# Performance work log

Measured on AMD Instinct MI355X. Metric: run time of the kernel, lower is better.

Reference implementation:

```python
import jax, jax.numpy as jnp
import numpy as np

N_NODES = 100000
N_TYPES = 7
E_PER_TYPE = 250000
D = 128


def setup_inputs() -> dict:
    key = jax.random.key(0)
    k1, k2, k3 = jax.random.split(key, 3)
    x = jax.random.normal(k1, (N_NODES, D), dtype=jnp.float32)
    edge_index = jax.random.randint(k2, (N_TYPES, 2, E_PER_TYPE), 0, N_NODES, dtype=jnp.int64)
    # per-edge-type GNN weights (SwitchModule holds one param set per type)
    W = jax.random.normal(k3, (N_TYPES, D, D), dtype=jnp.float32) * (1.0 / np.sqrt(D))
    b = jnp.zeros((N_TYPES, D), dtype=jnp.float32)
    return {"x": x, "edge_index": edge_index, "W": W, "b": b}


def reference(x, edge_index, W, b):
    # x: [N, D]; edge_index: [T, 2, E]; W: [T, D, D]; b: [T, D]
    N = x.shape[0]
    E = edge_index.shape[-1]
    # per-type linear transform of all node features: [T, N, D]
    h = jnp.einsum('nd,tdf->tnf', x, W) + b[:, None, :]

    def per_type(ht, ei):
        src, dst = ei[0], ei[1]
        msgs = ht[src]                                   # [E, D] gather
        sums = jax.ops.segment_sum(msgs, dst, num_segments=N)
        cnt = jax.ops.segment_sum(jnp.ones((E,), ht.dtype), dst, num_segments=N)
        return sums / jnp.maximum(cnt, 1.0)[:, None]     # mean aggregation

    type_messages = jax.vmap(per_type)(h, edge_index)    # [T, N, D]
    # x_agg = sum(type_messages) / len(type_messages)
    return type_messages.mean(axis=0)
```

## Files before the change

kernel.cpp:

```cpp
#include <hip/hip_runtime.h>


constexpr int NN = 100000;
constexpr int NT = 7;
constexpr int NE = 250000;
constexpr int DD = 128;
constexpr int NROWS = ((NN + 127) / 128) * 128;
constexpr int NPART = 8;
constexpr int PSIZE = (NN + NPART - 1) / NPART;
constexpr int EPB = 1024;
constexpr int NSLAB = (NE + EPB - 1) / EPB;

typedef short bf16x8 __attribute__((ext_vector_type(8)));
typedef float f32x4 __attribute__((ext_vector_type(4)));
typedef int   i32x4 __attribute__((ext_vector_type(4)));
typedef float fltx4 __attribute__((ext_vector_type(4)));

__device__ __forceinline__ unsigned pack_bf16x2(float lo, float hi) {
    unsigned a = __float_as_uint(lo), b = __float_as_uint(hi);
    unsigned al = (a + 0x7FFFu + ((a >> 16) & 1u)) >> 16;
    unsigned bh = (b + 0x7FFFu + ((b >> 16) & 1u)) & 0xFFFF0000u;
    return al | bh;
}

__global__ __launch_bounds__(256) void convx_k(
    const float* __restrict__ x, uint4* __restrict__ xb)
{
    int id = blockIdx.x * 256 + threadIdx.x;
    const fltx4* src = (const fltx4*)x;
    fltx4 v0 = __builtin_nontemporal_load(src + (size_t)id * 2);
    fltx4 v1 = __builtin_nontemporal_load(src + (size_t)id * 2 + 1);
    uint4 o;
    o.x = pack_bf16x2(v0[0], v0[1]);
    o.y = pack_bf16x2(v0[2], v0[3]);
    o.z = pack_bf16x2(v1[0], v1[1]);
    o.w = pack_bf16x2(v1[2], v1[3]);
    xb[id] = o;
}

__global__ __launch_bounds__(256) void wconv_k(
    const float* __restrict__ W, char* __restrict__ WTb)
{
    int wid = (blockIdx.x * 256 + threadIdx.x) >> 6;
    int lane = threadIdx.x & 63;
    int t = wid >> 7, f = wid & 127;
    if (t >= NT) return;
    const float* Wt = W + (size_t)t * DD * DD;
    float w0 = Wt[(size_t)(2 * lane) * DD + f];
    float w1 = Wt[(size_t)(2 * lane + 1) * DD + f];
    int gran = (lane >> 2) ^ (f & 7);
    *(unsigned*)(WTb + (size_t)t * 32768 + f * 256 + gran * 16 + (lane & 3) * 4)
        = pack_bf16x2(w0, w1);
}

__global__ __launch_bounds__(256) void fill_k(
    const int* __restrict__ ei,
    int* __restrict__ cntT,
    int* __restrict__ eslots)
{
    int part = blockIdx.x & (NPART - 1);
    int slab = blockIdx.x >> 3;
    int t = blockIdx.y;
    int e0 = slab * EPB + threadIdx.x * 4;
    if (e0 >= NE) return;
    const int* p = ei + (size_t)t * 2 * NE;
    i32x4 s4 = __builtin_nontemporal_load((const i32x4*)(p + e0));
    i32x4 d4 = __builtin_nontemporal_load((const i32x4*)(p + NE + e0));
    int lo = part * PSIZE;
    int hi = lo + PSIZE;
    int tv = t << 17;
    #pragma unroll
    for (int k = 0; k < 4; ++k) {
        int src = s4[k];
        int dst = d4[k];
        if (dst >= lo && dst < hi) {
            int pos = atomicAdd(cntT + dst, 1);
            if (pos < 64) eslots[(size_t)dst * 64 + pos] = src | tv;
        }
    }
}

__global__ __launch_bounds__(256) void agg_k(
    const char* __restrict__ xb,
    const int* __restrict__ cntT,
    const int* __restrict__ eslots,
    char* __restrict__ aggb,
    unsigned char* __restrict__ bmask,
    int c0, int nc)
{
    int wid = (blockIdx.x * 256 + threadIdx.x) >> 6;
    int lane = threadIdx.x & 63;
    if (wid >= nc) return;
    const int n = c0 + wid;
    const bool live = (n < NN);

    int total = live ? cntT[n] : 0;
    if (total > 64) total = 64;
    int val = (live && lane < total)
            ? __builtin_nontemporal_load(eslots + (size_t)n * 64 + lane) : 0;
    int mytype = (lane < total) ? ((val >> 17) & 7) : 7;

    unsigned long long bal[8];
    #pragma unroll
    for (int t = 0; t < 8; ++t) bal[t] = __ballot(mytype == t);
    int ct[7], st[7];
    {
        int s = 0;
        #pragma unroll
        for (int t = 0; t < 7; ++t) { st[t] = s; ct[t] = (int)__popcll(bal[t]); s += ct[t]; }
    }

    unsigned long long before = 0, mine = bal[7];
    #pragma unroll
    for (int t = 0; t < 7; ++t) {
        before |= (mytype > t) ? bal[t] : 0ull;
        mine = (mytype == t) ? bal[t] : mine;
    }
    int rank = (int)__popcll(before)
             + (int)__popcll(mine & ((1ull << lane) - 1ull));
    int sorted = __builtin_amdgcn_ds_permute(rank << 2, val);
    int val2 = (lane < total) ? (sorted & 0x1FFFF) : NN;

    int gran = (lane >> 2) ^ (wid & 7);
    char* wbase = aggb + (size_t)(wid >> 7) * 32768 + (size_t)(wid & 127) * 256
                + gran * 16 + (lane & 3) * 4;
    const size_t tstride = (size_t)nc * 256;
    unsigned msk = 0;

    #pragma unroll
    for (int tp = 0; tp < 7; tp += 2) {
        const int cA = ct[tp], stA = st[tp];
        const int cB = (tp + 1 < 7) ? ct[tp + 1] : 0;
        const int stB = (tp + 1 < 7) ? st[tp + 1] : 0;
        int m2 = cA > cB ? cA : cB;

        float a0 = 0.f, a1 = 0.f, b0 = 0.f, b1 = 0.f;
        for (int e = 0; e < m2; e += 2) {
            int iA0 = (e < cA)     ? stA + e     : 63;
            int iA1 = (e + 1 < cA) ? stA + e + 1 : 63;
            int iB0 = (e < cB)     ? stB + e     : 63;
            int iB1 = (e + 1 < cB) ? stB + e + 1 : 63;
            int sA0 = __shfl(val2, iA0);
            int sA1 = __shfl(val2, iA1);
            int sB0 = __shfl(val2, iB0);
            int sB1 = __shfl(val2, iB1);
            unsigned vA0 = *(const unsigned*)(xb + (size_t)sA0 * 256 + lane * 4);
            unsigned vA1 = *(const unsigned*)(xb + (size_t)sA1 * 256 + lane * 4);
            unsigned vB0 = *(const unsigned*)(xb + (size_t)sB0 * 256 + lane * 4);
            unsigned vB1 = *(const unsigned*)(xb + (size_t)sB1 * 256 + lane * 4);
            a0 += __uint_as_float(vA0 << 16) + __uint_as_float(vA1 << 16);
            a1 += __uint_as_float(vA0 & 0xFFFF0000u) + __uint_as_float(vA1 & 0xFFFF0000u);
            b0 += __uint_as_float(vB0 << 16) + __uint_as_float(vB1 << 16);
            b1 += __uint_as_float(vB0 & 0xFFFF0000u) + __uint_as_float(vB1 & 0xFFFF0000u);
        }
        float sa = 1.0f / fmaxf((float)cA, 1.0f);
        *(unsigned*)(wbase + (size_t)tp * tstride) = pack_bf16x2(a0 * sa, a1 * sa);
        msk |= (cA > 0) ? (1u << tp) : 0u;
        if (tp + 1 < 7) {
            float sb = 1.0f / fmaxf((float)cB, 1.0f);
            *(unsigned*)(wbase + (size_t)(tp + 1) * tstride) = pack_bf16x2(b0 * sb, b1 * sb);
            msk |= (cB > 0) ? (1u << (tp + 1)) : 0u;
        }
    }
    if (live && lane == 0) bmask[n] = (unsigned char)msk;
}

__global__ __launch_bounds__(512) void gemm_k(
    const char* __restrict__ aggb, const char* __restrict__ WTb,
    const unsigned char* __restrict__ bmask, const float* __restrict__ bias,
    float* __restrict__ out, int c0, int nc)
{
    __shared__ char sA[128 * 256];
    __shared__ char sW[128 * 256];
    int tid = threadIdx.x;
    int w = tid >> 6, lane = tid & 63;
    int wy = w >> 1, wx = w & 1;
    int n0 = c0 + blockIdx.x * 128;
    const size_t tstride = (size_t)nc * 256;

    f32x4 acc[2][4];
    #pragma unroll
    for (int i = 0; i < 2; ++i)
        #pragma unroll
        for (int j = 0; j < 4; ++j) acc[i][j] = (f32x4)0.0f;

    for (int t = 0; t < NT; ++t) {
        __syncthreads();
        const char* asrc = aggb + (size_t)t * tstride + (size_t)blockIdx.x * 32768;
        const char* wsrc = WTb + (size_t)t * 32768;
        #pragma unroll
        for (int i = 0; i < 4; ++i) {
            int ch = w * 4 + i;
            __builtin_amdgcn_global_load_lds(
                (const __attribute__((address_space(1))) void*)(asrc + ch * 1024 + lane * 16),
                (__attribute__((address_space(3))) void*)(sA + ch * 1024), 16, 0, 0);
            __builtin_amdgcn_global_load_lds(
                (const __attribute__((address_space(1))) void*)(wsrc + ch * 1024 + lane * 16),
                (__attribute__((address_space(3))) void*)(sW + ch * 1024), 16, 0, 0);
        }
        __syncthreads();

        #pragma unroll
        for (int c = 0; c < 4; ++c) {
            int gsel = ((c * 4 + (lane >> 4)) ^ (lane & 7)) << 4;
            bf16x8 A0 = *(const bf16x8*)(sA + (wy * 32 + (lane & 15)) * 256 + gsel);
            bf16x8 A1 = *(const bf16x8*)(sA + (wy * 32 + 16 + (lane & 15)) * 256 + gsel);
            #pragma unroll
            for (int nj = 0; nj < 4; ++nj) {
                bf16x8 B = *(const bf16x8*)(sW + (wx * 64 + nj * 16 + (lane & 15)) * 256 + gsel);
                acc[0][nj] = __builtin_amdgcn_mfma_f32_16x16x32_bf16(A0, B, acc[0][nj], 0, 0, 0);
                acc[1][nj] = __builtin_amdgcn_mfma_f32_16x16x32_bf16(A1, B, acc[1][nj], 0, 0, 0);
            }
        }
    }

    const float inv7 = 1.0f / (float)NT;
    #pragma unroll
    for (int mi = 0; mi < 2; ++mi) {
        #pragma unroll
        for (int v = 0; v < 4; ++v) {
            int n = n0 + wy * 32 + mi * 16 + (lane >> 4) * 4 + v;
            if (n >= NN) continue;
            unsigned mk = bmask[n];
            float add[4] = {0.f, 0.f, 0.f, 0.f};
            #pragma unroll
            for (int t = 0; t < NT; ++t) {
                if ((mk >> t) & 1u) {
                    #pragma unroll
                    for (int nj = 0; nj < 4; ++nj)
                        add[nj] += bias[(size_t)t * DD + wx * 64 + nj * 16 + (lane & 15)];
                }
            }
            #pragma unroll
            for (int nj = 0; nj < 4; ++nj)
                out[(size_t)n * DD + wx * 64 + nj * 16 + (lane & 15)]
                    = inv7 * (acc[mi][nj][v] + add[nj]);
        }
    }
}

extern "C" void kernel_launch(void* const* d_in, const int* in_sizes, int n_in,
                              void* d_out, int out_size, void* d_ws, size_t ws_size,
                              hipStream_t stream) {
    const float* x  = (const float*)d_in[0];
    const int*   ei = (const int*)d_in[1];
    const float* W  = (const float*)d_in[2];
    const float* b  = (const float*)d_in[3];
    float* out = (float*)d_out;
    char* ws = (char*)d_ws;

    size_t off = 0;
    char* xb     = ws + off; off += (size_t)(NN + 1) * 256;
    char* WTb    = ws + off; off += (size_t)NT * 128 * 256;
    int*  eslots = (int*)(ws + off); off += (size_t)NN * 64 * 4;
    int*  cntT   = (int*)(ws + off); off += (size_t)NN * 4;
    unsigned char* bmask = (unsigned char*)(ws + off); off += (size_t)NN;
    off = (off + 255) & ~(size_t)255;
    char* aggb   = ws + off;

    size_t avail = (ws_size > off) ? (ws_size - off) : 0;
    int Nc = (int)(avail / ((size_t)NT * 256));
    Nc &= ~127;
    if (Nc < 128) Nc = 128;
    if (Nc > NROWS) Nc = NROWS;

    convx_k<<<(NN * DD / 8 + 255) / 256, 256, 0, stream>>>(x, (uint4*)xb);
    hipMemsetAsync(xb + (size_t)NN * 256, 0, 256, stream);
    wconv_k<<<(NT * 128 + 3) / 4, 256, 0, stream>>>(W, WTb);
    hipMemsetAsync(cntT, 0, (size_t)NN * 4, stream);
    fill_k<<<dim3(NSLAB * NPART, NT), 256, 0, stream>>>(ei, cntT, eslots);

    for (int c0 = 0; c0 < NN; c0 += Nc) {
        int nc = (NROWS - c0 < Nc) ? (NROWS - c0) : Nc;
        agg_k<<<nc / 4, 256, 0, stream>>>(xb, cntT, eslots, aggb, bmask, c0, nc);
        gemm_k<<<nc / 128, 512, 0, stream>>>(aggb, WTb, bmask, b, out, c0, nc);
    }
}
```

Before: 257.4 us.

## Fuse per-type gather aggregation into GEMM kernel, removing intermediate agg buffer

Splits the old aggregation kernel in two. A sort kernel reorders each node's edge slots by type in place and packs per-type counts into a 64-bit word. A fused kernel then gathers the neighbour features for each type straight into LDS and runs the MFMA GEMM on them, so the bf16 aggregated buffer is never written to or read back from global memory and the chunk loop goes away. The cost is that gather latency now sits inside the GEMM kernel between barriers, with a large block, which may limit occupancy and latency hiding. The 512-thread block also gathers its rows serially, one wave per row.

```diff
diff --git a/kernel.cpp b/kernel.cpp
--- a/kernel.cpp
+++ b/kernel.cpp
@@ -80,34 +80,29 @@
     }
 }
 
-__global__ __launch_bounds__(256) void agg_k(
-    const char* __restrict__ xb,
+__global__ __launch_bounds__(256) void sort_k(
     const int* __restrict__ cntT,
-    const int* __restrict__ eslots,
-    char* __restrict__ aggb,
-    unsigned char* __restrict__ bmask,
-    int c0, int nc)
-{
-    int wid = (blockIdx.x * 256 + threadIdx.x) >> 6;
+    int* __restrict__ eslots,
+    unsigned long long* __restrict__ cntpack)
+{
+    int n = (blockIdx.x * 256 + threadIdx.x) >> 6;
     int lane = threadIdx.x & 63;
-    if (wid >= nc) return;
-    const int n = c0 + wid;
-    const bool live = (n < NN);
-
-    int total = live ? cntT[n] : 0;
+    if (n >= NN) return;
+
+    int total = cntT[n];
     if (total > 64) total = 64;
-    int val = (live && lane < total)
-            ? __builtin_nontemporal_load(eslots + (size_t)n * 64 + lane) : 0;
+    int val = (lane < total) ? eslots[(size_t)n * 64 + lane] : 0;
     int mytype = (lane < total) ? ((val >> 17) & 7) : 7;
 
     unsigned long long bal[8];
     #pragma unroll
     for (int t = 0; t < 8; ++t) bal[t] = __ballot(mytype == t);
-    int ct[7], st[7];
-    {
-        int s = 0;
-        #pragma unroll
-        for (int t = 0; t < 7; ++t) { st[t] = s; ct[t] = (int)__popcll(bal[t]); s += ct[t]; }
+    int ct[7];
+    unsigned long long pk = 0;
+    #pragma unroll
+    for (int t = 0; t < 7; ++t) {
+        ct[t] = (int)__popcll(bal[t]);
+        pk |= (unsigned long long)ct[t] << (8 * t);
     }
 
     unsigned long long before = 0, mine = bal[7];
@@ -119,64 +114,26 @@
     int rank = (int)__popcll(before)
              + (int)__popcll(mine & ((1ull << lane) - 1ull));
     int sorted = __builtin_amdgcn_ds_permute(rank << 2, val);
-    int val2 = (lane < total) ? (sorted & 0x1FFFF) : NN;
-
-    int gran = (lane >> 2) ^ (wid & 7);
-    char* wbase = aggb + (size_t)(wid >> 7) * 32768 + (size_t)(wid & 127) * 256
-                + gran * 16 + (lane & 3) * 4;
-    const size_t tstride = (size_t)nc * 256;
-    unsigned msk = 0;
-
-    #pragma unroll
-    for (int tp = 0; tp < 7; tp += 2) {
-        const int cA = ct[tp], stA = st[tp];
-        const int cB = (tp + 1 < 7) ? ct[tp + 1] : 0;
-        const int stB = (tp + 1 < 7) ? st[tp + 1] : 0;
-        int m2 = cA > cB ? cA : cB;
-
-        float a0 = 0.f, a1 = 0.f, b0 = 0.f, b1 = 0.f;
-        for (int e = 0; e < m2; e += 2) {
-            int iA0 = (e < cA)     ? stA + e     : 63;
-            int iA1 = (e + 1 < cA) ? stA + e + 1 : 63;
-            int iB0 = (e < cB)     ? stB + e     : 63;
-            int iB1 = (e + 1 < cB) ? stB + e + 1 : 63;
-            int sA0 = __shfl(val2, iA0);
-            int sA1 = __shfl(val2, iA1);
-            int sB0 = __shfl(val2, iB0);
-            int sB1 = __shfl(val2, iB1);
-            unsigned vA0 = *(const unsigned*)(xb + (size_t)sA0 * 256 + lane * 4);
-            unsigned vA1 = *(const unsigned*)(xb + (size_t)sA1 * 256 + lane * 4);
-            unsigned vB0 = *(const unsigned*)(xb + (size_t)sB0 * 256 + lane * 4);
-            unsigned vB1 = *(const unsigned*)(xb + (size_t)sB1 * 256 + lane * 4);
-            a0 += __uint_as_float(vA0 << 16) + __uint_as_float(vA1 << 16);
-            a1 += __uint_as_float(vA0 & 0xFFFF0000u) + __uint_as_float(vA1 & 0xFFFF0000u);
-            b0 += __uint_as_float(vB0 << 16) + __uint_as_float(vB1 << 16);
-            b1 += __uint_as_float(vB0 & 0xFFFF0000u) + __uint_as_float(vB1 & 0xFFFF0000u);
-        }
-        float sa = 1.0f / fmaxf((float)cA, 1.0f);
-        *(unsigned*)(wbase + (size_t)tp * tstride) = pack_bf16x2(a0 * sa, a1 * sa);
-        msk |= (cA > 0) ? (1u << tp) : 0u;
-        if (tp + 1 < 7) {
-            float sb = 1.0f / fmaxf((float)cB, 1.0f);
-            *(unsigned*)(wbase + (size_t)(tp + 1) * tstride) = pack_bf16x2(b0 * sb, b1 * sb);
-            msk |= (cB > 0) ? (1u << (tp + 1)) : 0u;
-        }
-    }
-    if (live && lane == 0) bmask[n] = (unsigned char)msk;
-}
-
-__global__ __launch_bounds__(512) void gemm_k(
-    const char* __restrict__ aggb, const char* __restrict__ WTb,
-    const unsigned char* __restrict__ bmask, const float* __restrict__ bias,
-    float* __restrict__ out, int c0, int nc)
+    int srcv = (lane < total) ? (sorted & 0x1FFFF) : NN;
+
+    eslots[(size_t)n * 64 + lane] = srcv;
+    if (lane == 0) cntpack[n] = pk;
+}
+
+__global__ __launch_bounds__(512) void fused_k(
+    const char* __restrict__ xb,
+    const int* __restrict__ eslots,
+    const unsigned long long* __restrict__ cntpack,
+    const char* __restrict__ WTb,
+    const float* __restrict__ bias,
+    float* __restrict__ out)
 {
     __shared__ char sA[128 * 256];
     __shared__ char sW[128 * 256];
     int tid = threadIdx.x;
     int w = tid >> 6, lane = tid & 63;
     int wy = w >> 1, wx = w & 1;
-    int n0 = c0 + blockIdx.x * 128;
-    const size_t tstride = (size_t)nc * 256;
+    int n0 = blockIdx.x * 128;
 
     f32x4 acc[2][4];
     #pragma unroll
@@ -186,23 +143,50 @@
 
     for (int t = 0; t < NT; ++t) {
         __syncthreads();
-        const char* asrc = aggb + (size_t)t * tstride + (size_t)blockIdx.x * 32768;
+
         const char* wsrc = WTb + (size_t)t * 32768;
         #pragma unroll
         for (int i = 0; i < 4; ++i) {
             int ch = w * 4 + i;
             __builtin_amdgcn_global_load_lds(
-                (const __attribute__((address_space(1))) void*)(asrc + ch * 1024 + lane * 16),
-                (__attribute__((address_space(3))) void*)(sA + ch * 1024), 16, 0, 0);
-            __builtin_amdgcn_global_load_lds(
                 (const __attribute__((address_space(1))) void*)(wsrc + ch * 1024 + lane * 16),
                 (__attribute__((address_space(3))) void*)(sW + ch * 1024), 16, 0, 0);
         }
+
+        for (int rr = 0; rr < 16; ++rr) {
+            int row = w * 16 + rr;
+            int node = n0 + row;
+            bool live = (node < NN);
+            int nn = live ? node : 0;
+            unsigned long long cp = live ? cntpack[nn] : 0ull;
+            int st = 0;
+            for (int u = 0; u < t; ++u) st += (int)((cp >> (8 * u)) & 0xFFull);
+            int c = (int)((cp >> (8 * t)) & 0xFFull);
+
+            int sidx = st + lane;
+            sidx = sidx < 63 ? sidx : 63;
+            int seg = eslots[(size_t)nn * 64 + sidx];
+
+            float a0 = 0.f, a1 = 0.f;
+            for (int e = 0; e < c; e += 2) {
+                int r0 = __shfl(seg, e);
+                int r1 = __shfl(seg, e + 1);
+                int s1 = (e + 1 < c) ? r1 : NN;
+                unsigned v0 = *(const unsigned*)(xb + (size_t)r0 * 256 + lane * 4);
+                unsigned v1 = *(const unsigned*)(xb + (size_t)s1 * 256 + lane * 4);
+                a0 += __uint_as_float(v0 << 16) + __uint_as_float(v1 << 16);
+                a1 += __uint_as_float(v0 & 0xFFFF0000u) + __uint_as_float(v1 & 0xFFFF0000u);
+            }
+            float sc = 1.0f / fmaxf((float)c, 1.0f);
+            int gran = (lane >> 2) ^ (row & 7);
+            *(unsigned*)(sA + row * 256 + gran * 16 + (lane & 3) * 4)
+                = pack_bf16x2(a0 * sc, a1 * sc);
+        }
         __syncthreads();
 
         #pragma unroll
-        for (int c = 0; c < 4; ++c) {
-            int gsel = ((c * 4 + (lane >> 4)) ^ (lane & 7)) << 4;
+        for (int cl = 0; cl < 4; ++cl) {
+            int gsel = ((cl * 4 + (lane >> 4)) ^ (lane & 7)) << 4;
             bf16x8 A0 = *(const bf16x8*)(sA + (wy * 32 + (lane & 15)) * 256 + gsel);
             bf16x8 A1 = *(const bf16x8*)(sA + (wy * 32 + 16 + (lane & 15)) * 256 + gsel);
             #pragma unroll
@@ -221,11 +205,11 @@
         for (int v = 0; v < 4; ++v) {
             int n = n0 + wy * 32 + mi * 16 + (lane >> 4) * 4 + v;
             if (n >= NN) continue;
-            unsigned mk = bmask[n];
+            unsigned long long cp = cntpack[n];
             float add[4] = {0.f, 0.f, 0.f, 0.f};
             #pragma unroll
             for (int t = 0; t < NT; ++t) {
-                if ((mk >> t) & 1u) {
+                if ((cp >> (8 * t)) & 0xFFull) {
                     #pragma unroll
                     for (int nj = 0; nj < 4; ++nj)
                         add[nj] += bias[(size_t)t * DD + wx * 64 + nj * 16 + (lane & 15)];
@@ -254,25 +238,14 @@
     char* WTb    = ws + off; off += (size_t)NT * 128 * 256;
     int*  eslots = (int*)(ws + off); off += (size_t)NN * 64 * 4;
     int*  cntT   = (int*)(ws + off); off += (size_t)NN * 4;
-    unsigned char* bmask = (unsigned char*)(ws + off); off += (size_t)NN;
-    off = (off + 255) & ~(size_t)255;
-    char* aggb   = ws + off;
-
-    size_t avail = (ws_size > off) ? (ws_size - off) : 0;
-    int Nc = (int)(avail / ((size_t)NT * 256));
-    Nc &= ~127;
-    if (Nc < 128) Nc = 128;
-    if (Nc > NROWS) Nc = NROWS;
+    unsigned long long* cntpack = (unsigned long long*)(ws + off);
+    off += (size_t)NN * 8;
 
     convx_k<<<(NN * DD / 8 + 255) / 256, 256, 0, stream>>>(x, (uint4*)xb);
     hipMemsetAsync(xb + (size_t)NN * 256, 0, 256, stream);
     wconv_k<<<(NT * 128 + 3) / 4, 256, 0, stream>>>(W, WTb);
     hipMemsetAsync(cntT, 0, (size_t)NN * 4, stream);
     fill_k<<<dim3(NSLAB * NPART, NT), 256, 0, stream>>>(ei, cntT, eslots);
-
-    for (int c0 = 0; c0 < NN; c0 += Nc) {
-        int nc = (NROWS - c0 < Nc) ? (NROWS - c0) : Nc;
-        agg_k<<<nc / 4, 256, 0, stream>>>(xb, cntT, eslots, aggb, bmask, c0, nc);
-        gemm_k<<<nc / 128, 512, 0, stream>>>(aggb, WTb, bmask, b, out, c0, nc);
-    }
-}
+    sort_k<<<(NN * 64 + 255) / 256, 256, 0, stream>>>(cntT, eslots, cntpack);
+    fused_k<<<NROWS / 128, 512, 0, stream>>>(xb, eslots, cntpack, WTb, b, out);
+}
```

Measured after the change: 481.6 us. 1.87x slower.
